# Kernel optimization log

Measured on AMD Instinct MI355X. Metric: run time of the kernel, lower is better.

## Reference

```python
import jax, jax.numpy as jnp
import numpy as np

B, S, H = 32, 2048, 1024

def setup_inputs() -> dict:
    key = jax.random.key(0)
    ks = jax.random.split(key, 8)
    scale = 1.0 / np.sqrt(H)
    return {
        "query": jax.random.normal(ks[0], (B, H), jnp.float32),
        "keys": jax.random.normal(ks[1], (B, S, H), jnp.float32),
        "Wa_w": jax.random.uniform(ks[2], (H, H), jnp.float32, -scale, scale),
        "Wa_b": jax.random.uniform(ks[3], (H,), jnp.float32, -scale, scale),
        "Ua_w": jax.random.uniform(ks[4], (H, H), jnp.float32, -scale, scale),
        "Ua_b": jax.random.uniform(ks[5], (H,), jnp.float32, -scale, scale),
        "Va_w": jax.random.uniform(ks[6], (1, H), jnp.float32, -scale, scale),
        "Va_b": jax.random.uniform(ks[7], (1,), jnp.float32, -scale, scale),
    }

def reference(query, keys, Wa_w, Wa_b, Ua_w, Ua_b, Va_w, Va_b):
    # q_proj: [B, 1, H]; k_proj: [B, S, H]
    q_proj = (jnp.einsum('bh,oh->bo', query, Wa_w) + Wa_b)[:, None, :]
    k_proj = jnp.einsum('bsh,oh->bso', keys, Ua_w) + Ua_b
    # scores: [B, S] via Va(tanh(...)).squeeze
    scores = jnp.einsum('bsh,h->bs', jnp.tanh(q_proj + k_proj), Va_w[0]) + Va_b[0]
    weights = jax.nn.softmax(scores, axis=1)[:, None, :]  # [B, 1, S]
    context = jnp.einsum('bqs,bsh->bqh', weights, keys)   # [B, 1, H]
    return (context, weights)
```

## Files before the change

### kernel.cpp

```cpp
#include <hip/hip_runtime.h>
#include <hip/hip_bf16.h>


#define BB 32
#define SS 2048
#define HH 1024

typedef float  f32x4  __attribute__((ext_vector_type(4)));
typedef __bf16 bf16x4 __attribute__((ext_vector_type(4)));
typedef __bf16 bf16x8 __attribute__((ext_vector_type(8)));

__device__ inline __bf16 f2bf(float f) {
  unsigned u = __builtin_bit_cast(unsigned, f);
  u = (u + 0x7FFFu + ((u >> 16) & 1u)) >> 16;
  unsigned short s = (unsigned short)u;
  return __builtin_bit_cast(__bf16, s);
}

__device__ inline float bf2f(__bf16 b) {
  unsigned short s = __builtin_bit_cast(unsigned short, b);
  unsigned u = ((unsigned)s) << 16;
  return __builtin_bit_cast(float, u);
}

__device__ inline float tanh_fast(float x) {
  x = fminf(fmaxf(x, -15.f), 15.f);
  float e = __expf(2.f * x);
  return (e - 1.f) / (e + 1.f);
}

__device__ __forceinline__ void gload16(const __bf16* g, __bf16* l) {
  __builtin_amdgcn_global_load_lds(
      (const __attribute__((address_space(1))) void*)g,
      (__attribute__((address_space(3))) void*)l, 16, 0, 0);
}

__global__ void k_convert_keys(const float* __restrict__ src, __bf16* __restrict__ dst) {
  size_t i = ((size_t)blockIdx.x * 256 + threadIdx.x) * 8;
  f32x4 a = *(const f32x4*)(src + i);
  f32x4 b = *(const f32x4*)(src + i + 4);
  bf16x8 o;
  o[0] = f2bf(a[0]); o[1] = f2bf(a[1]); o[2] = f2bf(a[2]); o[3] = f2bf(a[3]);
  o[4] = f2bf(b[0]); o[5] = f2bf(b[1]); o[6] = f2bf(b[2]); o[7] = f2bf(b[3]);
  *(bf16x8*)(dst + i) = o;
}

__global__ void k_convert_ua(const float* __restrict__ src, __bf16* __restrict__ dst) {
  size_t i = (size_t)blockIdx.x * 256 + threadIdx.x;
  f32x4 v = ((const f32x4*)src)[i];
  bf16x4 o;
  o[0] = f2bf(v[0]); o[1] = f2bf(v[1]); o[2] = f2bf(v[2]); o[3] = f2bf(v[3]);
  *(bf16x4*)(dst + i * 4) = o;
}

__global__ void k_qproj(const float* __restrict__ q, const float* __restrict__ wa,
                        const float* __restrict__ wab, const float* __restrict__ uab,
                        float* __restrict__ qpc) {
  int tid = threadIdx.x;
  int gid = blockIdx.x * 32 + (tid >> 3);
  int lane8 = tid & 7;
  int b = gid >> 10, o = gid & 1023;
  const f32x4* qv = (const f32x4*)(q + (size_t)b * HH);
  const f32x4* wv = (const f32x4*)(wa + (size_t)o * HH);
  float s = 0.f;
#pragma unroll 4
  for (int kk = lane8; kk < HH / 4; kk += 8) {
    f32x4 a = qv[kk], w = wv[kk];
    s += a[0] * w[0] + a[1] * w[1] + a[2] * w[2] + a[3] * w[3];
  }
  s += __shfl_xor(s, 1); s += __shfl_xor(s, 2); s += __shfl_xor(s, 4);
  if (lane8 == 0) qpc[(size_t)b * HH + o] = s + wab[o] + uab[o];
}

__global__ void __launch_bounds__(256) k_scores5(
    const __bf16* __restrict__ keysb, const __bf16* __restrict__ ua,
    const float* __restrict__ qpc, const float* __restrict__ vaw,
    float* __restrict__ spart) {
  __shared__ __align__(16) __bf16 Alds[128 * 64];
  __shared__ __align__(16) __bf16 Blds[128 * 64];
  __shared__ float scorebuf[128];

  int raw = blockIdx.x;
  int o = (raw >> 3) & 7;
  int m = ((raw >> 6) << 3) | (raw & 7);
  int b = m >> 4;
  long grow0 = (long)m * 128;
  int o0 = o * 128;

  int tid = threadIdx.x;
  int w = tid >> 6, lane = tid & 63;
  int wm = w >> 1, wn = w & 1;
  int ln = lane & 15, hi = lane >> 4;

  int srow = tid >> 3;
  int sslot = tid & 7;
  const __bf16 *ag0, *ag1, *ag2, *ag3, *bg0, *bg1, *bg2, *bg3;
  {
    int r0 = 0 * 32 + srow, r1 = 1 * 32 + srow, r2 = 2 * 32 + srow, r3 = 3 * 32 + srow;
    int g0 = (sslot - r0) & 7, g1 = (sslot - r1) & 7, g2 = (sslot - r2) & 7, g3 = (sslot - r3) & 7;
    ag0 = keysb + (size_t)(grow0 + r0) * HH + g0 * 8;
    ag1 = keysb + (size_t)(grow0 + r1) * HH + g1 * 8;
    ag2 = keysb + (size_t)(grow0 + r2) * HH + g2 * 8;
    ag3 = keysb + (size_t)(grow0 + r3) * HH + g3 * 8;
    bg0 = ua + (size_t)(o0 + r0) * HH + g0 * 8;
    bg1 = ua + (size_t)(o0 + r1) * HH + g1 * 8;
    bg2 = ua + (size_t)(o0 + r2) * HH + g2 * 8;
    bg3 = ua + (size_t)(o0 + r3) * HH + g3 * 8;
  }
  __bf16* al0 = Alds + 0 * 2048 + w * 512;
  __bf16* al1 = Alds + 1 * 2048 + w * 512;
  __bf16* al2 = Alds + 2 * 2048 + w * 512;
  __bf16* al3 = Alds + 3 * 2048 + w * 512;
  __bf16* bl0 = Blds + 0 * 2048 + w * 512;
  __bf16* bl1 = Blds + 1 * 2048 + w * 512;
  __bf16* bl2 = Blds + 2 * 2048 + w * 512;
  __bf16* bl3 = Blds + 3 * 2048 + w * 512;

  int ra = (wm * 64 + ln) * 64;
  int rb = (wn * 64 + ln) * 64;
  int sa0 = ((hi + ln) & 7) * 8;
  int sa1 = ((4 + hi + ln) & 7) * 8;

  f32x4 acc[4][4] = {};

  for (int kt = 0; kt < 16; ++kt) {
    if (kt) __syncthreads();
    int ko = kt * 64;
    gload16(ag0 + ko, al0); gload16(ag1 + ko, al1);
    gload16(ag2 + ko, al2); gload16(ag3 + ko, al3);
    gload16(bg0 + ko, bl0); gload16(bg1 + ko, bl1);
    gload16(bg2 + ko, bl2); gload16(bg3 + ko, bl3);
    __syncthreads();

    bf16x8 af[4], bfr[4];
#pragma unroll
    for (int mi = 0; mi < 4; ++mi)
      af[mi] = *(const bf16x8*)(Alds + ra + mi * 1024 + sa0);
#pragma unroll
    for (int ni = 0; ni < 4; ++ni)
      bfr[ni] = *(const bf16x8*)(Blds + rb + ni * 1024 + sa0);
#pragma unroll
    for (int mi = 0; mi < 4; ++mi)
#pragma unroll
      for (int ni = 0; ni < 4; ++ni)
        acc[mi][ni] = __builtin_amdgcn_mfma_f32_16x16x32_bf16(af[mi], bfr[ni], acc[mi][ni], 0, 0, 0);
#pragma unroll
    for (int mi = 0; mi < 4; ++mi)
      af[mi] = *(const bf16x8*)(Alds + ra + mi * 1024 + sa1);
#pragma unroll
    for (int ni = 0; ni < 4; ++ni)
      bfr[ni] = *(const bf16x8*)(Blds + rb + ni * 1024 + sa1);
#pragma unroll
    for (int mi = 0; mi < 4; ++mi)
#pragma unroll
      for (int ni = 0; ni < 4; ++ni)
        acc[mi][ni] = __builtin_amdgcn_mfma_f32_16x16x32_bf16(af[mi], bfr[ni], acc[mi][ni], 0, 0, 0);
  }

  float qv[4], vv[4];
#pragma unroll
  for (int ni = 0; ni < 4; ++ni) {
    int oc = o0 + wn * 64 + ni * 16 + ln;
    qv[ni] = qpc[(size_t)b * HH + oc];
    vv[ni] = vaw[oc];
  }
  float rsum[4][4];
#pragma unroll
  for (int mi = 0; mi < 4; ++mi)
#pragma unroll
    for (int j = 0; j < 4; ++j) {
      float v = 0.f;
#pragma unroll
      for (int ni = 0; ni < 4; ++ni)
        v += tanh_fast(acc[mi][ni][j] + qv[ni]) * vv[ni];
      v += __shfl_xor(v, 1); v += __shfl_xor(v, 2);
      v += __shfl_xor(v, 4); v += __shfl_xor(v, 8);
      rsum[mi][j] = v;
    }
  if (wn == 1 && ln == 0) {
#pragma unroll
    for (int mi = 0; mi < 4; ++mi)
#pragma unroll
      for (int j = 0; j < 4; ++j)
        scorebuf[wm * 64 + mi * 16 + hi * 4 + j] = rsum[mi][j];
  }
  __syncthreads();
  if (wn == 0 && ln == 0) {
#pragma unroll
    for (int mi = 0; mi < 4; ++mi)
#pragma unroll
      for (int j = 0; j < 4; ++j) {
        int rl = wm * 64 + mi * 16 + hi * 4 + j;
        spart[(size_t)o * (BB * SS) + grow0 + rl] = rsum[mi][j] + scorebuf[rl];
      }
  }
}

__global__ void __launch_bounds__(256) k_scores_fused(
    const float* __restrict__ keys, const __bf16* __restrict__ ua,
    const float* __restrict__ qpc, const float* __restrict__ vaw,
    float* __restrict__ spart) {
  __shared__ __bf16 Alds[128][40];
  __shared__ float scorebuf[128];

  int raw = blockIdx.x;
  int o = (raw >> 3) & 7;
  int m = ((raw >> 6) << 3) | (raw & 7);
  int b = m >> 4;
  long grow0 = (long)m * 128;
  int o0 = o * 128;

  int tid = threadIdx.x;
  int w = tid >> 6, lane = tid & 63;
  int wm = w >> 1, wn = w & 1;
  int ln = lane & 15, hi = lane >> 4;

  int srow = tid >> 3;
  int sk4 = tid & 7;
  const f32x4* keysv = (const f32x4*)keys;
  const bf16x8* uav = (const bf16x8*)ua;

  f32x4 acc[4][4] = {};

  for (int kt = 0; kt < 32; ++kt) {
    int k0 = kt * 32;
    bf16x8 bf[4];
#pragma unroll
    for (int ni = 0; ni < 4; ++ni) {
      int oc = o0 + wn * 64 + ni * 16 + ln;
      bf[ni] = uav[(size_t)oc * (HH / 8) + (k0 >> 3) + hi];
    }
    f32x4 st[4];
#pragma unroll
    for (int p = 0; p < 4; ++p)
      st[p] = keysv[((size_t)(grow0 + srow + 32 * p) << 8) + (size_t)(kt * 8 + sk4)];
    __syncthreads();
#pragma unroll
    for (int p = 0; p < 4; ++p) {
      bf16x4 t;
      t[0] = f2bf(st[p][0]); t[1] = f2bf(st[p][1]);
      t[2] = f2bf(st[p][2]); t[3] = f2bf(st[p][3]);
      *(bf16x4*)&Alds[srow + 32 * p][sk4 * 4] = t;
    }
    __syncthreads();
    bf16x8 af[4];
#pragma unroll
    for (int mi = 0; mi < 4; ++mi)
      af[mi] = *(const bf16x8*)&Alds[wm * 64 + mi * 16 + ln][hi * 8];
#pragma unroll
    for (int mi = 0; mi < 4; ++mi)
#pragma unroll
      for (int ni = 0; ni < 4; ++ni)
        acc[mi][ni] = __builtin_amdgcn_mfma_f32_16x16x32_bf16(af[mi], bf[ni], acc[mi][ni], 0, 0, 0);
  }

  float qv[4], vv[4];
#pragma unroll
  for (int ni = 0; ni < 4; ++ni) {
    int oc = o0 + wn * 64 + ni * 16 + ln;
    qv[ni] = qpc[(size_t)b * HH + oc];
    vv[ni] = vaw[oc];
  }
  float rsum[4][4];
#pragma unroll
  for (int mi = 0; mi < 4; ++mi)
#pragma unroll
    for (int j = 0; j < 4; ++j) {
      float v = 0.f;
#pragma unroll
      for (int ni = 0; ni < 4; ++ni)
        v += tanh_fast(acc[mi][ni][j] + qv[ni]) * vv[ni];
      v += __shfl_xor(v, 1); v += __shfl_xor(v, 2);
      v += __shfl_xor(v, 4); v += __shfl_xor(v, 8);
      rsum[mi][j] = v;
    }
  if (wn == 1 && ln == 0) {
#pragma unroll
    for (int mi = 0; mi < 4; ++mi)
#pragma unroll
      for (int j = 0; j < 4; ++j)
        scorebuf[wm * 64 + mi * 16 + hi * 4 + j] = rsum[mi][j];
  }
  __syncthreads();
  if (wn == 0 && ln == 0) {
#pragma unroll
    for (int mi = 0; mi < 4; ++mi)
#pragma unroll
      for (int j = 0; j < 4; ++j) {
        int rl = wm * 64 + mi * 16 + hi * 4 + j;
        spart[(size_t)o * (BB * SS) + grow0 + rl] = rsum[mi][j] + scorebuf[rl];
      }
  }
}

__global__ void k_softmax(const float* __restrict__ spart, float* __restrict__ wout) {
  int b = blockIdx.x, tid = threadIdx.x;
  __shared__ float red[8];
  int w = tid >> 6;
  float sc[8];
  float mx = -1e30f;
#pragma unroll
  for (int i = 0; i < 8; ++i) {
    int s = tid + i * 256;
    float v = 0.f;
#pragma unroll
    for (int ot = 0; ot < 8; ++ot) v += spart[(size_t)ot * (BB * SS) + b * SS + s];
    sc[i] = v; mx = fmaxf(mx, v);
  }
#pragma unroll
  for (int off = 1; off < 64; off <<= 1) mx = fmaxf(mx, __shfl_xor(mx, off));
  if ((tid & 63) == 0) red[w] = mx;
  __syncthreads();
  mx = fmaxf(fmaxf(red[0], red[1]), fmaxf(red[2], red[3]));
  float sum = 0.f;
#pragma unroll
  for (int i = 0; i < 8; ++i) { sc[i] = __expf(sc[i] - mx); sum += sc[i]; }
#pragma unroll
  for (int off = 1; off < 64; off <<= 1) sum += __shfl_xor(sum, off);
  if ((tid & 63) == 0) red[4 + w] = sum;
  __syncthreads();
  sum = (red[4] + red[5]) + (red[6] + red[7]);
  float inv = 1.f / sum;
#pragma unroll
  for (int i = 0; i < 8; ++i) wout[(size_t)b * SS + tid + i * 256] = sc[i] * inv;
}

__global__ void k_ctx_part_bf(const __bf16* __restrict__ keysb, const float* __restrict__ wts,
                              float* __restrict__ cpart) {
  int bc = blockIdx.x;
  int b = bc >> 4, sc = bc & 15;
  int tid = threadIdx.x;
  int s0 = sc * 128;
  f32x4 a0 = {0,0,0,0}, a1 = {0,0,0,0}, a2 = {0,0,0,0}, a3 = {0,0,0,0};
  for (int s = 0; s < 128; s += 4) {
    size_t base = (size_t)b * SS + s0 + s;
    float w0 = wts[base + 0], w1 = wts[base + 1], w2 = wts[base + 2], w3 = wts[base + 3];
    bf16x4 k0 = *(const bf16x4*)(keysb + (base + 0) * HH + tid * 4);
    bf16x4 k1 = *(const bf16x4*)(keysb + (base + 1) * HH + tid * 4);
    bf16x4 k2 = *(const bf16x4*)(keysb + (base + 2) * HH + tid * 4);
    bf16x4 k3 = *(const bf16x4*)(keysb + (base + 3) * HH + tid * 4);
#pragma unroll
    for (int j = 0; j < 4; ++j) {
      a0[j] += w0 * bf2f(k0[j]);
      a1[j] += w1 * bf2f(k1[j]);
      a2[j] += w2 * bf2f(k2[j]);
      a3[j] += w3 * bf2f(k3[j]);
    }
  }
  f32x4 a = (a0 + a1) + (a2 + a3);
  ((f32x4*)cpart)[(size_t)bc * (HH / 4) + tid] = a;
}

__global__ void k_ctx_part(const float* __restrict__ keys, const float* __restrict__ wts,
                           float* __restrict__ cpart) {
  int bc = blockIdx.x;
  int b = bc >> 4, sc = bc & 15;
  int tid = threadIdx.x;
  int s0 = sc * 128;
  const f32x4* kv = (const f32x4*)keys;
  f32x4 a0 = {0,0,0,0}, a1 = {0,0,0,0}, a2 = {0,0,0,0}, a3 = {0,0,0,0};
  for (int s = 0; s < 128; s += 4) {
    size_t base = (size_t)b * SS + s0 + s;
    a0 += wts[base + 0] * kv[(base + 0) * (HH / 4) + tid];
    a1 += wts[base + 1] * kv[(base + 1) * (HH / 4) + tid];
    a2 += wts[base + 2] * kv[(base + 2) * (HH / 4) + tid];
    a3 += wts[base + 3] * kv[(base + 3) * (HH / 4) + tid];
  }
  f32x4 a = (a0 + a1) + (a2 + a3);
  ((f32x4*)cpart)[(size_t)bc * (HH / 4) + tid] = a;
}

__global__ void k_ctx_red(const float* __restrict__ cpart, float* __restrict__ ctx) {
  int i = blockIdx.x * 256 + threadIdx.x;
  int b = i >> 10, h = i & 1023;
  float v = 0.f;
#pragma unroll
  for (int sc = 0; sc < 16; ++sc) v += cpart[((size_t)(b * 16 + sc)) * HH + h];
  ctx[i] = v;
}

extern "C" void kernel_launch(void* const* d_in, const int* in_sizes, int n_in,
                              void* d_out, int out_size, void* d_ws, size_t ws_size,
                              hipStream_t stream) {
  (void)in_sizes; (void)n_in; (void)out_size;
  const float* query = (const float*)d_in[0];
  const float* keys  = (const float*)d_in[1];
  const float* wa_w  = (const float*)d_in[2];
  const float* wa_b  = (const float*)d_in[3];
  const float* ua_w  = (const float*)d_in[4];
  const float* ua_b  = (const float*)d_in[5];
  const float* va_w  = (const float*)d_in[6];

  char* ws = (char*)d_ws;
  float* ctx_out = (float*)d_out;
  float* w_out   = ctx_out + BB * HH;

  const size_t need = (size_t)135 << 20;
  if (ws_size >= need) {
    __bf16* keys_bf = (__bf16*)ws;
    __bf16* ua_bf   = (__bf16*)(ws + ((size_t)128 << 20));
    float*  qpc     = (float*)(ws + ((size_t)130 << 20));
    float*  spart   = (float*)(ws + ((size_t)131 << 20));
    float*  cpart   = (float*)(ws + ((size_t)133 << 20));

    k_convert_keys<<<BB * SS * HH / (256 * 8), 256, 0, stream>>>(keys, keys_bf);
    k_convert_ua<<<1024, 256, 0, stream>>>(ua_w, ua_bf);
    k_qproj<<<1024, 256, 0, stream>>>(query, wa_w, wa_b, ua_b, qpc);
    k_scores5<<<4096, 256, 0, stream>>>(keys_bf, ua_bf, qpc, va_w, spart);
    k_softmax<<<BB, 256, 0, stream>>>(spart, w_out);
    k_ctx_part_bf<<<512, 256, 0, stream>>>(keys_bf, w_out, cpart);
    k_ctx_red<<<BB * HH / 256, 256, 0, stream>>>(cpart, ctx_out);
  } else {
    __bf16* ua_bf  = (__bf16*)ws;
    float*  qpc    = (float*)(ws + (2u << 20));
    float*  spart  = (float*)(ws + (2u << 20) + (128u << 10));
    float*  cpart  = (float*)(ws + (4u << 20) + (128u << 10));

    k_convert_ua<<<1024, 256, 0, stream>>>(ua_w, ua_bf);
    k_qproj<<<1024, 256, 0, stream>>>(query, wa_w, wa_b, ua_b, qpc);
    k_scores_fused<<<4096, 256, 0, stream>>>(keys, ua_bf, qpc, va_w, spart);
    k_softmax<<<BB, 256, 0, stream>>>(spart, w_out);
    k_ctx_part<<<512, 256, 0, stream>>>(keys, w_out, cpart);
    k_ctx_red<<<BB * HH / 256, 256, 0, stream>>>(cpart, ctx_out);
  }
}
```

Before: 258.2 us.

## Double-buffer LDS tiles in scores GEMM and prefetch next k-tile

The scores GEMM kernel now keeps two LDS buffers for the A and B tiles and issues the direct-to-LDS loads for tile k+1 before computing on tile k. It waits with a partial vmcnt so only the current tile's loads must finish, and raises wave priority around the MFMA blocks. The goal is to overlap global-memory latency with matrix math instead of serialising load and compute each iteration. In exchange LDS use doubles, which may lower occupancy, and the final iteration issues one redundant reload of tile 15.

New measurement: 306.2 us. 1.19x slower.

```diff
diff --git a/kernel.cpp b/kernel.cpp
--- a/kernel.cpp
+++ b/kernel.cpp
@@ -72,12 +72,12 @@
   if (lane8 == 0) qpc[(size_t)b * HH + o] = s + wab[o] + uab[o];
 }
 
-__global__ void __launch_bounds__(256) k_scores5(
+__global__ void __launch_bounds__(256) k_scores6(
     const __bf16* __restrict__ keysb, const __bf16* __restrict__ ua,
     const float* __restrict__ qpc, const float* __restrict__ vaw,
     float* __restrict__ spart) {
-  __shared__ __align__(16) __bf16 Alds[128 * 64];
-  __shared__ __align__(16) __bf16 Blds[128 * 64];
+  __shared__ __align__(16) __bf16 Alds[2][128 * 64];
+  __shared__ __align__(16) __bf16 Blds[2][128 * 64];
   __shared__ float scorebuf[128];
 
   int raw = blockIdx.x;
@@ -107,14 +107,20 @@
     bg2 = ua + (size_t)(o0 + r2) * HH + g2 * 8;
     bg3 = ua + (size_t)(o0 + r3) * HH + g3 * 8;
   }
-  __bf16* al0 = Alds + 0 * 2048 + w * 512;
-  __bf16* al1 = Alds + 1 * 2048 + w * 512;
-  __bf16* al2 = Alds + 2 * 2048 + w * 512;
-  __bf16* al3 = Alds + 3 * 2048 + w * 512;
-  __bf16* bl0 = Blds + 0 * 2048 + w * 512;
-  __bf16* bl1 = Blds + 1 * 2048 + w * 512;
-  __bf16* bl2 = Blds + 2 * 2048 + w * 512;
-  __bf16* bl3 = Blds + 3 * 2048 + w * 512;
+  int wofs = w * 512;
+
+#define STAGE6(kn, bi)                                         \
+  do {                                                         \
+    int ko_ = (kn)*64;                                         \
+    gload16(ag0 + ko_, &Alds[bi][0 * 2048 + wofs]);            \
+    gload16(ag1 + ko_, &Alds[bi][1 * 2048 + wofs]);            \
+    gload16(ag2 + ko_, &Alds[bi][2 * 2048 + wofs]);            \
+    gload16(ag3 + ko_, &Alds[bi][3 * 2048 + wofs]);            \
+    gload16(bg0 + ko_, &Blds[bi][0 * 2048 + wofs]);            \
+    gload16(bg1 + ko_, &Blds[bi][1 * 2048 + wofs]);            \
+    gload16(bg2 + ko_, &Blds[bi][2 * 2048 + wofs]);            \
+    gload16(bg3 + ko_, &Blds[bi][3 * 2048 + wofs]);            \
+  } while (0)
 
   int ra = (wm * 64 + ln) * 64;
   int rb = (wn * 64 + ln) * 64;
@@ -123,39 +129,50 @@
 
   f32x4 acc[4][4] = {};
 
+  STAGE6(0, 0);
+
   for (int kt = 0; kt < 16; ++kt) {
-    if (kt) __syncthreads();
-    int ko = kt * 64;
-    gload16(ag0 + ko, al0); gload16(ag1 + ko, al1);
-    gload16(ag2 + ko, al2); gload16(ag3 + ko, al3);
-    gload16(bg0 + ko, bl0); gload16(bg1 + ko, bl1);
-    gload16(bg2 + ko, bl2); gload16(bg3 + ko, bl3);
-    __syncthreads();
-
+    __builtin_amdgcn_s_barrier();
+    __builtin_amdgcn_sched_barrier(0);
+    STAGE6(kt + 1 < 16 ? kt + 1 : 15, (kt + 1) & 1);
+    __builtin_amdgcn_sched_barrier(0);
+    asm volatile("s_waitcnt vmcnt(8)" ::: "memory");
+    __builtin_amdgcn_sched_barrier(0);
+    __builtin_amdgcn_s_barrier();
+    __builtin_amdgcn_sched_barrier(0);
+
+    const __bf16* Ab = &Alds[kt & 1][0];
+    const __bf16* Bb = &Blds[kt & 1][0];
     bf16x8 af[4], bfr[4];
 #pragma unroll
     for (int mi = 0; mi < 4; ++mi)
-      af[mi] = *(const bf16x8*)(Alds + ra + mi * 1024 + sa0);
+      af[mi] = *(const bf16x8*)(Ab + ra + mi * 1024 + sa0);
 #pragma unroll
     for (int ni = 0; ni < 4; ++ni)
-      bfr[ni] = *(const bf16x8*)(Blds + rb + ni * 1024 + sa0);
+      bfr[ni] = *(const bf16x8*)(Bb + rb + ni * 1024 + sa0);
+    __builtin_amdgcn_s_setprio(1);
 #pragma unroll
     for (int mi = 0; mi < 4; ++mi)
 #pragma unroll
       for (int ni = 0; ni < 4; ++ni)
         acc[mi][ni] = __builtin_amdgcn_mfma_f32_16x16x32_bf16(af[mi], bfr[ni], acc[mi][ni], 0, 0, 0);
-#pragma unroll
-    for (int mi = 0; mi < 4; ++mi)
-      af[mi] = *(const bf16x8*)(Alds + ra + mi * 1024 + sa1);
+    __builtin_amdgcn_s_setprio(0);
+#pragma unroll
+    for (int mi = 0; mi < 4; ++mi)
+      af[mi] = *(const bf16x8*)(Ab + ra + mi * 1024 + sa1);
 #pragma unroll
     for (int ni = 0; ni < 4; ++ni)
-      bfr[ni] = *(const bf16x8*)(Blds + rb + ni * 1024 + sa1);
+      bfr[ni] = *(const bf16x8*)(Bb + rb + ni * 1024 + sa1);
+    __builtin_amdgcn_s_setprio(1);
 #pragma unroll
     for (int mi = 0; mi < 4; ++mi)
 #pragma unroll
       for (int ni = 0; ni < 4; ++ni)
         acc[mi][ni] = __builtin_amdgcn_mfma_f32_16x16x32_bf16(af[mi], bfr[ni], acc[mi][ni], 0, 0, 0);
-  }
+    __builtin_amdgcn_s_setprio(0);
+    __builtin_amdgcn_sched_barrier(0);
+  }
+#undef STAGE6
 
   float qv[4], vv[4];
 #pragma unroll
@@ -406,7 +423,7 @@
     k_convert_keys<<<BB * SS * HH / (256 * 8), 256, 0, stream>>>(keys, keys_bf);
     k_convert_ua<<<1024, 256, 0, stream>>>(ua_w, ua_bf);
     k_qproj<<<1024, 256, 0, stream>>>(query, wa_w, wa_b, ua_b, qpc);
-    k_scores5<<<4096, 256, 0, stream>>>(keys_bf, ua_bf, qpc, va_w, spart);
+    k_scores6<<<4096, 256, 0, stream>>>(keys_bf, ua_bf, qpc, va_w, spart);
     k_softmax<<<BB, 256, 0, stream>>>(spart, w_out);
     k_ctx_part_bf<<<512, 256, 0, stream>>>(keys_bf, w_out, cpart);
     k_ctx_red<<<BB * HH / 256, 256, 0, stream>>>(cpart, ctx_out);
```

## Fuse fp32-to-bf16 key conversion into the scores GEMM A-tile load

Applied to the files above, without the earlier changes.

Removes the separate key conversion kernel. The scores GEMM now reads fp32 keys directly, converts them to bf16 in registers and writes them to LDS. Blocks with output tile o==0 also write the bf16 keys to global memory for the later context kernel. This drops one full fp32 read and bf16 write pass over the keys, but each of the 8 output-column tiles now reads fp32 keys (twice the bytes of bf16) through synchronous register loads instead of async global_load_lds, which may expose more load latency.

Measured after the change: 346.6 us. 1.34x slower.

```diff
diff --git a/kernel.cpp b/kernel.cpp
--- a/kernel.cpp
+++ b/kernel.cpp
@@ -33,16 +33,6 @@
   __builtin_amdgcn_global_load_lds(
       (const __attribute__((address_space(1))) void*)g,
       (__attribute__((address_space(3))) void*)l, 16, 0, 0);
-}
-
-__global__ void k_convert_keys(const float* __restrict__ src, __bf16* __restrict__ dst) {
-  size_t i = ((size_t)blockIdx.x * 256 + threadIdx.x) * 8;
-  f32x4 a = *(const f32x4*)(src + i);
-  f32x4 b = *(const f32x4*)(src + i + 4);
-  bf16x8 o;
-  o[0] = f2bf(a[0]); o[1] = f2bf(a[1]); o[2] = f2bf(a[2]); o[3] = f2bf(a[3]);
-  o[4] = f2bf(b[0]); o[5] = f2bf(b[1]); o[6] = f2bf(b[2]); o[7] = f2bf(b[3]);
-  *(bf16x8*)(dst + i) = o;
 }
 
 __global__ void k_convert_ua(const float* __restrict__ src, __bf16* __restrict__ dst) {
@@ -72,10 +62,10 @@
   if (lane8 == 0) qpc[(size_t)b * HH + o] = s + wab[o] + uab[o];
 }
 
-__global__ void __launch_bounds__(256) k_scores5(
-    const __bf16* __restrict__ keysb, const __bf16* __restrict__ ua,
+__global__ void __launch_bounds__(256) k_scores9(
+    const float* __restrict__ keysf, const __bf16* __restrict__ ua,
     const float* __restrict__ qpc, const float* __restrict__ vaw,
-    float* __restrict__ spart) {
+    __bf16* __restrict__ kbf_out, float* __restrict__ spart) {
   __shared__ __align__(16) __bf16 Alds[128 * 64];
   __shared__ __align__(16) __bf16 Blds[128 * 64];
   __shared__ float scorebuf[128];
@@ -92,25 +82,25 @@
   int wm = w >> 1, wn = w & 1;
   int ln = lane & 15, hi = lane >> 4;
 
+  int arow_s = w * 4 + (lane >> 4);
+  int akidx = (lane & 15) * 4;
+  const float* afp = keysf + (size_t)(grow0 + arow_s) * HH + akidx;
+  int aslot = (((lane & 15) >> 1) + arow_s) & 7;
+  int asub = lane & 1;
+  int awofs = arow_s * 64 + aslot * 8 + asub * 4;
+  __bf16* kout = kbf_out + (size_t)(grow0 + arow_s) * HH + akidx;
+
   int srow = tid >> 3;
   int sslot = tid & 7;
-  const __bf16 *ag0, *ag1, *ag2, *ag3, *bg0, *bg1, *bg2, *bg3;
+  const __bf16 *bg0, *bg1, *bg2, *bg3;
   {
     int r0 = 0 * 32 + srow, r1 = 1 * 32 + srow, r2 = 2 * 32 + srow, r3 = 3 * 32 + srow;
     int g0 = (sslot - r0) & 7, g1 = (sslot - r1) & 7, g2 = (sslot - r2) & 7, g3 = (sslot - r3) & 7;
-    ag0 = keysb + (size_t)(grow0 + r0) * HH + g0 * 8;
-    ag1 = keysb + (size_t)(grow0 + r1) * HH + g1 * 8;
-    ag2 = keysb + (size_t)(grow0 + r2) * HH + g2 * 8;
-    ag3 = keysb + (size_t)(grow0 + r3) * HH + g3 * 8;
     bg0 = ua + (size_t)(o0 + r0) * HH + g0 * 8;
     bg1 = ua + (size_t)(o0 + r1) * HH + g1 * 8;
     bg2 = ua + (size_t)(o0 + r2) * HH + g2 * 8;
     bg3 = ua + (size_t)(o0 + r3) * HH + g3 * 8;
   }
-  __bf16* al0 = Alds + 0 * 2048 + w * 512;
-  __bf16* al1 = Alds + 1 * 2048 + w * 512;
-  __bf16* al2 = Alds + 2 * 2048 + w * 512;
-  __bf16* al3 = Alds + 3 * 2048 + w * 512;
   __bf16* bl0 = Blds + 0 * 2048 + w * 512;
   __bf16* bl1 = Blds + 1 * 2048 + w * 512;
   __bf16* bl2 = Blds + 2 * 2048 + w * 512;
@@ -126,10 +116,24 @@
   for (int kt = 0; kt < 16; ++kt) {
     if (kt) __syncthreads();
     int ko = kt * 64;
-    gload16(ag0 + ko, al0); gload16(ag1 + ko, al1);
-    gload16(ag2 + ko, al2); gload16(ag3 + ko, al3);
     gload16(bg0 + ko, bl0); gload16(bg1 + ko, bl1);
     gload16(bg2 + ko, bl2); gload16(bg3 + ko, bl3);
+#pragma unroll
+    for (int h = 0; h < 2; ++h) {
+      f32x4 fa[4];
+#pragma unroll
+      for (int j = 0; j < 4; ++j)
+        fa[j] = *(const f32x4*)(afp + (size_t)(h * 4 + j) * 16 * HH + ko);
+#pragma unroll
+      for (int j = 0; j < 4; ++j) {
+        bf16x4 v;
+        v[0] = f2bf(fa[j][0]); v[1] = f2bf(fa[j][1]);
+        v[2] = f2bf(fa[j][2]); v[3] = f2bf(fa[j][3]);
+        *(bf16x4*)(Alds + (h * 4 + j) * 1024 + awofs) = v;
+        if (o == 0)
+          *(bf16x4*)(kout + (size_t)(h * 4 + j) * 16 * HH + ko) = v;
+      }
+    }
     __syncthreads();
 
     bf16x8 af[4], bfr[4];
@@ -403,10 +407,9 @@
     float*  spart   = (float*)(ws + ((size_t)131 << 20));
     float*  cpart   = (float*)(ws + ((size_t)133 << 20));
 
-    k_convert_keys<<<BB * SS * HH / (256 * 8), 256, 0, stream>>>(keys, keys_bf);
+    k_qproj<<<1024, 256, 0, stream>>>(query, wa_w, wa_b, ua_b, qpc);
     k_convert_ua<<<1024, 256, 0, stream>>>(ua_w, ua_bf);
-    k_qproj<<<1024, 256, 0, stream>>>(query, wa_w, wa_b, ua_b, qpc);
-    k_scores5<<<4096, 256, 0, stream>>>(keys_bf, ua_bf, qpc, va_w, spart);
+    k_scores9<<<4096, 256, 0, stream>>>(keys, ua_bf, qpc, va_w, keys_bf, spart);
     k_softmax<<<BB, 256, 0, stream>>>(spart, w_out);
     k_ctx_part_bf<<<512, 256, 0, stream>>>(keys_bf, w_out, cpart);
     k_ctx_red<<<BB * HH / 256, 256, 0, stream>>>(cpart, ctx_out);
```
